# Kernel optimization log

Hardware: AMD Instinct MI355X
Metric: run time of the kernel (lower is better)

Reference implementation:

```python
import jax, jax.numpy as jnp
import numpy as np

N_EMBD = 768
NUM_EXPERTS = 64
EXPERT_WIDTH = 256            # all experts uniform width (expert_sizes=[(64,256)])
TOTAL_WIDTH = NUM_EXPERTS * EXPERT_WIDTH  # 16384
TOP_K = 8


def setup_inputs() -> dict:
    key = jax.random.key(0)
    k1, k2, k3, k4 = jax.random.split(key, 4)
    B, S = 1, 2048
    x = jax.random.normal(k1, (B, S, N_EMBD), dtype=jnp.float32)
    # router: nn.Linear(n_embd, num_experts, bias=False) -> weight [E, n_embd]
    router_w = jax.random.normal(k2, (NUM_EXPERTS, N_EMBD), dtype=jnp.float32) * 0.02
    # trunc_normal(std=0.02) approximated by clipped normal
    w1 = jnp.clip(jax.random.normal(k3, (N_EMBD, TOTAL_WIDTH), dtype=jnp.float32) * 0.02, -0.06, 0.06)
    w2 = jnp.clip(jax.random.normal(k4, (TOTAL_WIDTH, N_EMBD), dtype=jnp.float32) * 0.02, -0.06, 0.06)
    return {"x": x, "router_w": router_w, "w1": w1, "w2": w2}


def reference(x, router_w, w1, w2):
    B, S, D = x.shape
    T = B * S
    x_flat = x.reshape(T, D)

    # Router: sigmoid gating + top-k
    router_logits = x_flat @ router_w.T                      # [T, E]
    router_probs = jax.nn.sigmoid(router_logits.astype(jnp.float32))
    top_k_weights, selected_experts = jax.lax.top_k(router_probs, TOP_K)  # [T, K]
    top_k_weights = top_k_weights / (top_k_weights.sum(axis=-1, keepdims=True) + 1e-20)
    top_k_weights = top_k_weights.astype(x.dtype)

    # Per-token expert combine weights [T, E]: 0 for unselected experts.
    tok_idx = jnp.arange(T)[:, None]
    w_tok = jnp.zeros((T, NUM_EXPERTS), dtype=x.dtype).at[tok_idx, selected_experts].set(top_k_weights)

    # Expert MLP (relu^2 activation), dense-masked equivalent of
    # padded_gather -> grouped GEMM -> padded_scatter.
    h = jnp.square(jax.nn.relu(x_flat @ w1))                 # [T, E*W]
    h = (h.reshape(T, NUM_EXPERTS, EXPERT_WIDTH) * w_tok[:, :, None]).reshape(T, TOTAL_WIDTH)
    output = (h @ w2).reshape(B, S, D)

    # Aux losses
    router_z_loss = jnp.mean(jnp.square(jax.nn.logsumexp(router_logits, axis=-1)))
    tokens_per_expert = jnp.zeros((NUM_EXPERTS,), dtype=jnp.float32).at[selected_experts.reshape(-1)].add(1.0)
    f_i = (tokens_per_expert / tokens_per_expert.sum()).astype(x.dtype)
    p_i = router_probs.mean(axis=0)
    # all expert widths equal -> num_experts * (f_i . p_i)
    load_balance_loss = NUM_EXPERTS * (f_i.astype(jnp.float32) @ p_i)
    # expert_widths_normalized == ones -> mean over tokens of sum of probs
    compute_loss = router_probs.sum(axis=-1).mean()

    return output, router_z_loss, load_balance_loss, compute_loss, f_i
```

## Files before the change

kernel.cpp:

```cpp
#include <hip/hip_runtime.h>
#include <hip/hip_bf16.h>

#define T_TOKENS 2048
#define D_EMBD 768
#define N_EXP 64
#define EW 256
#define TOPK 8
#define TW (N_EXP*EW)
#define PAD_SLOTS 20480
#define SCHED_MAX 2560
#define OUT_BASE (2048*768)

typedef __attribute__((ext_vector_type(8))) short bf16x8;
typedef __attribute__((ext_vector_type(4))) float f32x4;

typedef __attribute__((address_space(1))) void GAS;
typedef __attribute__((address_space(3))) void LAS;
#define GLOAD16(g, l) __builtin_amdgcn_global_load_lds((GAS*)(g), (LAS*)(l), 16, 0, 0)

__device__ inline unsigned short f2bu(float f) {
  union { __hip_bfloat16 b; unsigned short u; } cv; cv.b = __float2bfloat16(f); return cv.u;
}
__device__ inline unsigned int pk2(float a, float b) {
  return (unsigned int)f2bu(a) | ((unsigned int)f2bu(b) << 16);
}

__global__ void k_init(int* counts, int* cursor, float* psum, float* scal,
                       float* wgt_slot, int* tok_slot, int* sched_e) {
  int i = blockIdx.x*256 + threadIdx.x;
  if (i < N_EXP) { counts[i] = 0; cursor[i] = 0; psum[i] = 0.f; }
  if (i < 2) scal[i] = 0.f;
  if (i < PAD_SLOTS) { wgt_slot[i] = 0.f; tok_slot[i] = 0; }
  if (i < SCHED_MAX) sched_e[i] = -1;
}

__global__ __launch_bounds__(256) void k_logits(const float* __restrict__ x,
                                                const float* __restrict__ rw,
                                                float* __restrict__ lp) {
  __shared__ float rw_s[8][256];
  int tid = threadIdx.x;
  int tg = blockIdx.x, eg = blockIdx.y, kc = blockIdx.z;
  #pragma unroll
  for (int idx = 0; idx < 8; idx++)
    rw_s[idx][tid] = rw[(size_t)(eg*8 + idx)*D_EMBD + kc*256 + tid];
  __syncthreads();
  int tok = tg*256 + tid;
  const float4* x4 = reinterpret_cast<const float4*>(x + (size_t)tok*D_EMBD + kc*256);
  float acc[8];
  #pragma unroll
  for (int e = 0; e < 8; e++) acc[e] = 0.f;
  #pragma unroll 4
  for (int k4 = 0; k4 < 64; k4++) {
    float4 xv = x4[k4];
    #pragma unroll
    for (int e = 0; e < 8; e++)
      acc[e] += xv.x*rw_s[e][k4*4+0] + xv.y*rw_s[e][k4*4+1]
              + xv.z*rw_s[e][k4*4+2] + xv.w*rw_s[e][k4*4+3];
  }
  float* dst = lp + (size_t)kc*T_TOKENS*N_EXP + (size_t)tok*N_EXP + eg*8;
  float4 o0 = {acc[0], acc[1], acc[2], acc[3]};
  float4 o1 = {acc[4], acc[5], acc[6], acc[7]};
  reinterpret_cast<float4*>(dst)[0] = o0;
  reinterpret_cast<float4*>(dst)[1] = o1;
}

__global__ __launch_bounds__(256) void k_router2(const float* __restrict__ lp,
                          int* __restrict__ sel_e, float* __restrict__ sel_w,
                          int* __restrict__ counts, float* __restrict__ psum,
                          float* __restrict__ scal) {
  __shared__ float psum_s[4][64];
  __shared__ int cnt_s[4][64];
  int tid = threadIdx.x, wv = tid >> 6, lane = tid & 63;
  float pacc = 0.f, zacc = 0.f;
  int cacc = 0;
  int tbase = blockIdx.x*8 + wv*2;
  #pragma unroll
  for (int it = 0; it < 2; it++) {
    int t = tbase + it;
    float logit = lp[(size_t)t*N_EXP + lane]
                + lp[(size_t)T_TOKENS*N_EXP + (size_t)t*N_EXP + lane]
                + lp[2*(size_t)T_TOKENS*N_EXP + (size_t)t*N_EXP + lane];
    float prob = 1.f/(1.f + expf(-logit));
    pacc += prob;
    float mx = logit;
    for (int s = 32; s; s >>= 1) mx = fmaxf(mx, __shfl_xor(mx, s, 64));
    float sse = expf(logit - mx);
    for (int s = 32; s; s >>= 1) sse += __shfl_xor(sse, s, 64);
    float lse = mx + logf(sse);
    zacc += lse*lse;
    int rank = 0;
    #pragma unroll
    for (int j = 0; j < 64; j++) {
      float pj = __shfl(prob, j, 64);
      rank += (pj > prob || (pj == prob && j < lane)) ? 1 : 0;
    }
    bool sel = rank < TOPK;
    float sp = sel ? prob : 0.f;
    for (int s = 32; s; s >>= 1) sp += __shfl_xor(sp, s, 64);
    if (sel) {
      sel_e[t*TOPK + rank] = lane;
      sel_w[t*TOPK + rank] = prob / (sp + 1e-20f);
      cacc++;
    }
  }
  psum_s[wv][lane] = pacc;
  cnt_s[wv][lane] = cacc;
  if (lane == 0) atomicAdd(&scal[0], zacc);
  __syncthreads();
  if (tid < 64) {
    float p = psum_s[0][tid] + psum_s[1][tid] + psum_s[2][tid] + psum_s[3][tid];
    int c = cnt_s[0][tid] + cnt_s[1][tid] + cnt_s[2][tid] + cnt_s[3][tid];
    atomicAdd(&psum[tid], p);
    atomicAdd(&counts[tid], c);
  }
}

__global__ void k_schedule(const int* __restrict__ counts, int* __restrict__ offsets,
                           int* __restrict__ sched_e, int* __restrict__ sched_r0) {
  int e = threadIdx.x;
  int c = counts[e];
  int tiles = (c + 63) >> 6;
  int padded = tiles << 6;
  int ip = padded;
  for (int s = 1; s < 64; s <<= 1) { int v = __shfl_up(ip, s, 64); if (e >= s) ip += v; }
  int rowoff = ip - padded;
  offsets[e] = rowoff;
  int it = tiles;
  for (int s = 8; s < 64; s <<= 1) { int v = __shfl_up(it, s, 64); if (e >= s) it += v; }
  int rank = it - tiles;
  int xcd = e & 7;
  for (int i = 0; i < tiles; i++) {
    int p = xcd + 8*(rank + i);
    sched_e[p] = e;
    sched_r0[p] = rowoff + i*64;
  }
}

__global__ void k_assign(const int* __restrict__ sel_e, const float* __restrict__ sel_w,
                         const int* __restrict__ offsets, int* __restrict__ cursor,
                         int* __restrict__ tok_slot, float* __restrict__ wgt_slot,
                         int* __restrict__ slot_tk) {
  int i = blockIdx.x*256 + threadIdx.x;
  int e = sel_e[i];
  int pos = atomicAdd(&cursor[e], 1);
  int slot = offsets[e] + pos;
  tok_slot[slot] = i >> 3;
  wgt_slot[slot] = sel_w[i];
  slot_tk[i] = slot;
}

template<int MODE>
__global__ __launch_bounds__(256) void k_moe_gemm(
    const void* __restrict__ Asrc, const float* __restrict__ Bsrc,
    const int* __restrict__ sched_e, const int* __restrict__ sched_r0,
    const int* __restrict__ tok_slot, const float* __restrict__ wgt_slot,
    __hip_bfloat16* __restrict__ outp) {
  constexpr int NS   = (MODE == 1) ? 12 : 4;
  constexpr int BSTR = (MODE == 1) ? TW : D_EMBD;
  __shared__ __hip_bfloat16 As[2][64*64];
  __shared__ __hip_bfloat16 Bs[2][128*64];
  int tid = threadIdx.x;
  int nch = blockIdx.y;
  int n4 = tid & 31, kpb = tid >> 5;
  int mrow = tid >> 4, k4f = tid & 15;
  int arl = tid >> 3, akc = tid & 7;
  int a_off = ((akc ^ (arl & 7)) << 3);
  int wv = tid >> 6, lane = tid & 63;
  int wm = wv >> 1, wn = wv & 1;
  int l15 = lane & 15, l4 = lane >> 4;

  for (int p = blockIdx.x; p < SCHED_MAX; p += gridDim.x) {
    int e = sched_e[p];
    if (e < 0) continue;
    int r0 = sched_r0[p];

    int browb = (MODE == 1) ? 0 : e*EW;
    int bcolb = (MODE == 1) ? (e*EW + nch*128) : nch*128;

    int tks[4];
    size_t a_base0 = 0, a_base1 = 0;
    if (MODE == 1) {
      #pragma unroll
      for (int i = 0; i < 4; i++) tks[i] = tok_slot[r0 + i*16 + mrow];
    } else {
      a_base0 = (size_t)(r0 + arl) * EW;
      a_base1 = (size_t)(r0 + arl + 32) * EW;
    }

    float bv[8][4], av[4][4];

    auto B_LOAD = [&](int k0) {
      const float* rp = Bsrc + (size_t)(browb + k0 + kpb*8)*BSTR + bcolb + n4*4;
      #pragma unroll
      for (int r = 0; r < 8; r++)
        *reinterpret_cast<float4*>(&bv[r][0]) =
            *reinterpret_cast<const float4*>(rp + (size_t)r*BSTR);
    };
    auto B_WRITE = [&](int bsel) {
      char* bs = (char*)&Bs[bsel][0];
      #pragma unroll
      for (int c = 0; c < 4; c++) {
        int n = n4*4 + c;
        int ch = kpb ^ ((n & 7) ^ ((n >> 3) & 7));
        uint4 o = { pk2(bv[0][c], bv[1][c]), pk2(bv[2][c], bv[3][c]),
                    pk2(bv[4][c], bv[5][c]), pk2(bv[6][c], bv[7][c]) };
        *reinterpret_cast<uint4*>(bs + n*128 + ch*16) = o;
      }
    };
    auto A_LOAD1 = [&](int k0) {
      const float* xf = (const float*)Asrc;
      #pragma unroll
      for (int i = 0; i < 4; i++)
        *reinterpret_cast<float4*>(&av[i][0]) =
            *reinterpret_cast<const float4*>(xf + (size_t)tks[i]*D_EMBD + k0 + k4f*4);
    };
    auto A_WRITE1 = [&](int bsel) {
      char* as_ = (char*)&As[bsel][0];
      #pragma unroll
      for (int i = 0; i < 4; i++) {
        int m = i*16 + mrow;
        int ch = (k4f >> 1) ^ (m & 7);
        uint2 val = { pk2(av[i][0], av[i][1]), pk2(av[i][2], av[i][3]) };
        *reinterpret_cast<uint2*>(as_ + m*128 + ch*16 + (k4f & 1)*8) = val;
      }
    };
    auto A_GLOAD2 = [&](int bsel, int k0) {
      const __hip_bfloat16* hb = (const __hip_bfloat16*)Asrc;
      GLOAD16(hb + a_base0 + k0 + a_off, &As[bsel][0] + tid*8);
      GLOAD16(hb + a_base1 + k0 + a_off, &As[bsel][0] + (256 + tid)*8);
    };

    f32x4 acc[2][4];
    f32x4 z = {0.f, 0.f, 0.f, 0.f};
    #pragma unroll
    for (int m = 0; m < 2; m++)
      #pragma unroll
      for (int n = 0; n < 4; n++) acc[m][n] = z;

    if (MODE == 1) { A_LOAD1(0); B_LOAD(0); A_WRITE1(0); B_WRITE(0); }
    else           { A_GLOAD2(0, 0); B_LOAD(0); B_WRITE(0);
                     asm volatile("s_waitcnt vmcnt(0)" ::: "memory"); }
    __syncthreads();

    int cur = 0;
    for (int step = 0; step < NS; step++) {
      bool more = (step + 1 < NS);
      int k1 = (step + 1)*64;
      if (more) {
        if (MODE == 1) { A_LOAD1(k1); B_LOAD(k1); }
        else           { A_GLOAD2(cur ^ 1, k1); B_LOAD(k1); }
      }
      const char* asC = (const char*)&As[cur][0];
      const char* bsC = (const char*)&Bs[cur][0];
      bf16x8 af[2][2], bq[4][2];
      #pragma unroll
      for (int m = 0; m < 2; m++) {
        int ra = wm*32 + m*16 + l15;
        #pragma unroll
        for (int kk = 0; kk < 2; kk++)
          af[m][kk] = *reinterpret_cast<const bf16x8*>(
              asC + ra*128 + (((kk*4 + l4) ^ (ra & 7)) << 4));
      }
      #pragma unroll
      for (int n = 0; n < 4; n++) {
        int rb = wn*64 + n*16 + l15;
        int Sb = (rb & 7) ^ ((rb >> 3) & 7);
        #pragma unroll
        for (int kk = 0; kk < 2; kk++)
          bq[n][kk] = *reinterpret_cast<const bf16x8*>(
              bsC + rb*128 + (((kk*4 + l4) ^ Sb) << 4));
      }
      #pragma unroll
      for (int kk = 0; kk < 2; kk++)
        #pragma unroll
        for (int m = 0; m < 2; m++)
          #pragma unroll
          for (int n = 0; n < 4; n++)
            acc[m][n] = __builtin_amdgcn_mfma_f32_16x16x32_bf16(af[m][kk], bq[n][kk], acc[m][n], 0, 0, 0);
      if (more) {
        if (MODE == 1) { A_WRITE1(cur ^ 1); B_WRITE(cur ^ 1); }
        else           { B_WRITE(cur ^ 1);
                         asm volatile("s_waitcnt vmcnt(0)" ::: "memory"); }
      }
      __syncthreads();
      cur ^= 1;
    }

    if (MODE == 1) {
      #pragma unroll
      for (int m = 0; m < 2; m++)
        #pragma unroll
        for (int j = 0; j < 4; j++) {
          int r = r0 + wm*32 + m*16 + l4*4 + j;
          float wg = wgt_slot[r];
          #pragma unroll
          for (int n = 0; n < 4; n++) {
            int col = nch*128 + wn*64 + n*16 + l15;
            float v = fmaxf(acc[m][n][j], 0.f);
            outp[(size_t)r*EW + col] = __float2bfloat16(v*v*wg);
          }
        }
    } else {
      #pragma unroll
      for (int m = 0; m < 2; m++)
        #pragma unroll
        for (int j = 0; j < 4; j++) {
          int r = r0 + wm*32 + m*16 + l4*4 + j;
          #pragma unroll
          for (int n = 0; n < 4; n++) {
            int col = nch*128 + wn*64 + n*16 + l15;
            outp[(size_t)r*D_EMBD + col] = __float2bfloat16(acc[m][n][j]);
          }
        }
    }
  }
}

__global__ void k_combine(const __hip_bfloat16* __restrict__ y, const int* __restrict__ slot_tk,
                          float* __restrict__ out) {
  __shared__ int s[TOPK];
  int t = blockIdx.x, tid = threadIdx.x;
  if (tid < TOPK) s[tid] = slot_tk[t*TOPK + tid];
  __syncthreads();
  if (tid < 192) {
    int c = tid*4;
    float a0 = 0.f, a1 = 0.f, a2 = 0.f, a3 = 0.f;
    #pragma unroll
    for (int k = 0; k < TOPK; k++) {
      ushort4 v = *reinterpret_cast<const ushort4*>(&y[(size_t)s[k]*D_EMBD + c]);
      union { unsigned int u; float f; } f0, f1, f2, f3;
      f0.u = ((unsigned int)v.x) << 16;
      f1.u = ((unsigned int)v.y) << 16;
      f2.u = ((unsigned int)v.z) << 16;
      f3.u = ((unsigned int)v.w) << 16;
      a0 += f0.f; a1 += f1.f; a2 += f2.f; a3 += f3.f;
    }
    float4 o = {a0, a1, a2, a3};
    *reinterpret_cast<float4*>(&out[(size_t)t*D_EMBD + c]) = o;
  }
}

__global__ void k_finalize(const int* __restrict__ counts, const float* __restrict__ psum,
                           const float* __restrict__ scal, float* __restrict__ out) {
  __shared__ float part[N_EXP], ptot[N_EXP];
  int e = threadIdx.x;
  float f = (float)counts[e] / 16384.f;
  float p = psum[e] / 2048.f;
  part[e] = f * p;
  ptot[e] = p;
  out[OUT_BASE + 3 + e] = f;
  __syncthreads();
  if (e == 0) {
    float s = 0.f, q = 0.f;
    for (int i = 0; i < N_EXP; i++) { s += part[i]; q += ptot[i]; }
    out[OUT_BASE + 0] = scal[0] / 2048.f;
    out[OUT_BASE + 1] = 64.f * s;
    out[OUT_BASE + 2] = q;
  }
}

extern "C" void kernel_launch(void* const* d_in, const int* in_sizes, int n_in,
                              void* d_out, int out_size, void* d_ws, size_t ws_size,
                              hipStream_t stream) {
  const float* x  = (const float*)d_in[0];
  const float* rw = (const float*)d_in[1];
  const float* w1 = (const float*)d_in[2];
  const float* w2 = (const float*)d_in[3];
  float* out = (float*)d_out;
  char* ws = (char*)d_ws;

  size_t o = 0;
  auto alloc = [&](size_t b) { size_t r = o; o += (b + 255) & ~(size_t)255; return r; };
  __hip_bfloat16* hprm  = (__hip_bfloat16*)(ws + alloc((size_t)PAD_SLOTS*256*2));
  __hip_bfloat16* yprm  = (__hip_bfloat16*)(ws + alloc((size_t)PAD_SLOTS*768*2));
  float* lp      = (float*)(ws + alloc(3UL*2048*64*4));
  int*   sel_e   = (int*)  (ws + alloc(16384UL*4));
  float* sel_w   = (float*)(ws + alloc(16384UL*4));
  int*   slot_tk = (int*)  (ws + alloc(16384UL*4));
  int*   tokslot = (int*)  (ws + alloc((size_t)PAD_SLOTS*4));
  float* wgtslot = (float*)(ws + alloc((size_t)PAD_SLOTS*4));
  int*   counts  = (int*)  (ws + alloc(256));
  int*   cursor  = (int*)  (ws + alloc(256));
  float* psum    = (float*)(ws + alloc(256));
  float* scal    = (float*)(ws + alloc(256));
  int*   offsets = (int*)  (ws + alloc(256));
  int*   sch_e   = (int*)  (ws + alloc(SCHED_MAX*4));
  int*   sch_r0  = (int*)  (ws + alloc(SCHED_MAX*4));

  k_init<<<80, 256, 0, stream>>>(counts, cursor, psum, scal, wgtslot, tokslot, sch_e);
  k_logits<<<dim3(8, 8, 3), 256, 0, stream>>>(x, rw, lp);
  k_router2<<<256, 256, 0, stream>>>(lp, sel_e, sel_w, counts, psum, scal);
  k_schedule<<<1, 64, 0, stream>>>(counts, offsets, sch_e, sch_r0);
  k_assign<<<64, 256, 0, stream>>>(sel_e, sel_w, offsets, cursor, tokslot, wgtslot, slot_tk);
  k_moe_gemm<1><<<dim3(512, 2), 256, 0, stream>>>((const void*)x, w1, sch_e, sch_r0, tokslot, wgtslot, hprm);
  k_moe_gemm<2><<<dim3(512, 6), 256, 0, stream>>>((const void*)hprm, w2, sch_e, sch_r0, tokslot, wgtslot, yprm);
  k_combine<<<2048, 256, 0, stream>>>(yprm, slot_tk, out);
  k_finalize<<<1, 64, 0, stream>>>(counts, psum, scal, out);
}
```

Before: 141.7 us.

## Deepen GEMM prefetch to two register stages and drop direct global-to-LDS loads

The MoE grouped-GEMM main loop now keeps two sets of register staging buffers, so global loads are issued two K-steps ahead while the current LDS tile is computed. The loop is manually unrolled by two and fully unrolled. The bf16 A-operand path now does ordinary register loads plus LDS stores instead of global_load_lds, which removes the blocking vmcnt(0) wait after each step. The cost is much higher register pressure, which may lower occupancy or cause spills.

```diff
diff --git a/kernel.cpp b/kernel.cpp
--- a/kernel.cpp
+++ b/kernel.cpp
@@ -13,10 +13,6 @@
 
 typedef __attribute__((ext_vector_type(8))) short bf16x8;
 typedef __attribute__((ext_vector_type(4))) float f32x4;
-
-typedef __attribute__((address_space(1))) void GAS;
-typedef __attribute__((address_space(3))) void LAS;
-#define GLOAD16(g, l) __builtin_amdgcn_global_load_lds((GAS*)(g), (LAS*)(l), 16, 0, 0)
 
 __device__ inline unsigned short f2bu(float f) {
   union { __hip_bfloat16 b; unsigned short u; } cv; cv.b = __float2bfloat16(f); return cv.u;
@@ -187,16 +183,18 @@
       a_base1 = (size_t)(r0 + arl + 32) * EW;
     }
 
-    float bv[8][4], av[4][4];
-
-    auto B_LOAD = [&](int k0) {
+    float av0[4][4], av1[4][4];
+    uint4 au0[2], au1[2];
+    float bv0_[8][4], bv1_[8][4];
+
+    auto B_LD = [&](float (&bv)[8][4], int k0) {
       const float* rp = Bsrc + (size_t)(browb + k0 + kpb*8)*BSTR + bcolb + n4*4;
       #pragma unroll
       for (int r = 0; r < 8; r++)
         *reinterpret_cast<float4*>(&bv[r][0]) =
             *reinterpret_cast<const float4*>(rp + (size_t)r*BSTR);
     };
-    auto B_WRITE = [&](int bsel) {
+    auto B_WR = [&](int bsel, float (&bv)[8][4]) {
       char* bs = (char*)&Bs[bsel][0];
       #pragma unroll
       for (int c = 0; c < 4; c++) {
@@ -207,14 +205,14 @@
         *reinterpret_cast<uint4*>(bs + n*128 + ch*16) = o;
       }
     };
-    auto A_LOAD1 = [&](int k0) {
+    auto A_LD1 = [&](float (&av)[4][4], int k0) {
       const float* xf = (const float*)Asrc;
       #pragma unroll
       for (int i = 0; i < 4; i++)
         *reinterpret_cast<float4*>(&av[i][0]) =
             *reinterpret_cast<const float4*>(xf + (size_t)tks[i]*D_EMBD + k0 + k4f*4);
     };
-    auto A_WRITE1 = [&](int bsel) {
+    auto A_WR1 = [&](int bsel, float (&av)[4][4]) {
       char* as_ = (char*)&As[bsel][0];
       #pragma unroll
       for (int i = 0; i < 4; i++) {
@@ -224,10 +222,15 @@
         *reinterpret_cast<uint2*>(as_ + m*128 + ch*16 + (k4f & 1)*8) = val;
       }
     };
-    auto A_GLOAD2 = [&](int bsel, int k0) {
+    auto A_LD2 = [&](uint4 (&au)[2], int k0) {
       const __hip_bfloat16* hb = (const __hip_bfloat16*)Asrc;
-      GLOAD16(hb + a_base0 + k0 + a_off, &As[bsel][0] + tid*8);
-      GLOAD16(hb + a_base1 + k0 + a_off, &As[bsel][0] + (256 + tid)*8);
+      au[0] = *reinterpret_cast<const uint4*>(hb + a_base0 + k0 + a_off);
+      au[1] = *reinterpret_cast<const uint4*>(hb + a_base1 + k0 + a_off);
+    };
+    auto A_WR2 = [&](int bsel, uint4 (&au)[2]) {
+      char* as_ = (char*)&As[bsel][0];
+      *reinterpret_cast<uint4*>(as_ + tid*16) = au[0];
+      *reinterpret_cast<uint4*>(as_ + 4096 + tid*16) = au[1];
     };
 
     f32x4 acc[2][4];
@@ -237,21 +240,9 @@
       #pragma unroll
       for (int n = 0; n < 4; n++) acc[m][n] = z;
 
-    if (MODE == 1) { A_LOAD1(0); B_LOAD(0); A_WRITE1(0); B_WRITE(0); }
-    else           { A_GLOAD2(0, 0); B_LOAD(0); B_WRITE(0);
-                     asm volatile("s_waitcnt vmcnt(0)" ::: "memory"); }
-    __syncthreads();
-
-    int cur = 0;
-    for (int step = 0; step < NS; step++) {
-      bool more = (step + 1 < NS);
-      int k1 = (step + 1)*64;
-      if (more) {
-        if (MODE == 1) { A_LOAD1(k1); B_LOAD(k1); }
-        else           { A_GLOAD2(cur ^ 1, k1); B_LOAD(k1); }
-      }
-      const char* asC = (const char*)&As[cur][0];
-      const char* bsC = (const char*)&Bs[cur][0];
+    auto COMPUTE = [&](int bsel) {
+      const char* asC = (const char*)&As[bsel][0];
+      const char* bsC = (const char*)&Bs[bsel][0];
       bf16x8 af[2][2], bq[4][2];
       #pragma unroll
       for (int m = 0; m < 2; m++) {
@@ -277,10 +268,38 @@
           #pragma unroll
           for (int n = 0; n < 4; n++)
             acc[m][n] = __builtin_amdgcn_mfma_f32_16x16x32_bf16(af[m][kk], bq[n][kk], acc[m][n], 0, 0, 0);
-      if (more) {
-        if (MODE == 1) { A_WRITE1(cur ^ 1); B_WRITE(cur ^ 1); }
-        else           { B_WRITE(cur ^ 1);
-                         asm volatile("s_waitcnt vmcnt(0)" ::: "memory"); }
+    };
+
+    if (MODE == 1) A_LD1(av0, 0); else A_LD2(au0, 0);
+    B_LD(bv0_, 0);
+    if (MODE == 1) A_LD1(av1, 64); else A_LD2(au1, 64);
+    B_LD(bv1_, 64);
+    if (MODE == 1) A_WR1(0, av0); else A_WR2(0, au0);
+    B_WR(0, bv0_);
+    __syncthreads();
+
+    int cur = 0;
+    #pragma unroll
+    for (int t = 0; t < NS; t += 2) {
+      if (t + 2 < NS) {
+        if (MODE == 1) A_LD1(av0, (t+2)*64); else A_LD2(au0, (t+2)*64);
+        B_LD(bv0_, (t+2)*64);
+      }
+      COMPUTE(cur);
+      if (t + 1 < NS) {
+        if (MODE == 1) A_WR1(cur ^ 1, av1); else A_WR2(cur ^ 1, au1);
+        B_WR(cur ^ 1, bv1_);
+      }
+      __syncthreads();
+      cur ^= 1;
+      if (t + 3 < NS) {
+        if (MODE == 1) A_LD1(av1, (t+3)*64); else A_LD2(au1, (t+3)*64);
+        B_LD(bv1_, (t+3)*64);
+      }
+      COMPUTE(cur);
+      if (t + 2 < NS) {
+        if (MODE == 1) A_WR1(cur ^ 1, av0); else A_WR2(cur ^ 1, au0);
+        B_WR(cur ^ 1, bv0_);
       }
       __syncthreads();
       cur ^= 1;
```

Result: slower. 149.7 us (+5.7%).

## Group expert tiles per XCD contiguously and replace LDS-direct loads with register staging

Applied to the files above, without the earlier changes.

The schedule now gives each group of eight experts a contiguous segment of GRP_POS slots. Each block handles slots from its XCD's segment, so one XCD processes whole experts and reuses their weights in its L2. The MODE 2 A-operand load no longer uses global_load_lds with an explicit vmcnt wait. It loads into registers and writes to LDS after the MFMAs, the same way the B path does. This may improve L2 locality and overlap, but load balance across XCDs now depends on routing skew between expert groups.

```diff
diff --git a/kernel.cpp b/kernel.cpp
--- a/kernel.cpp
+++ b/kernel.cpp
@@ -9,14 +9,11 @@
 #define TW (N_EXP*EW)
 #define PAD_SLOTS 20480
 #define SCHED_MAX 2560
+#define GRP_POS 320
 #define OUT_BASE (2048*768)
 
 typedef __attribute__((ext_vector_type(8))) short bf16x8;
 typedef __attribute__((ext_vector_type(4))) float f32x4;
-
-typedef __attribute__((address_space(1))) void GAS;
-typedef __attribute__((address_space(3))) void LAS;
-#define GLOAD16(g, l) __builtin_amdgcn_global_load_lds((GAS*)(g), (LAS*)(l), 16, 0, 0)
 
 __device__ inline unsigned short f2bu(float f) {
   union { __hip_bfloat16 b; unsigned short u; } cv; cv.b = __float2bfloat16(f); return cv.u;
@@ -126,11 +123,11 @@
   int rowoff = ip - padded;
   offsets[e] = rowoff;
   int it = tiles;
-  for (int s = 8; s < 64; s <<= 1) { int v = __shfl_up(it, s, 64); if (e >= s) it += v; }
+  for (int s = 1; s < 8; s <<= 1) { int v = __shfl_up(it, s, 64); if ((e & 7) >= s) it += v; }
   int rank = it - tiles;
-  int xcd = e & 7;
+  int grp = e >> 3;
   for (int i = 0; i < tiles; i++) {
-    int p = xcd + 8*(rank + i);
+    int p = grp*GRP_POS + rank + i;
     sched_e[p] = e;
     sched_r0[p] = rowoff + i*64;
   }
@@ -169,7 +166,10 @@
   int wm = wv >> 1, wn = wv & 1;
   int l15 = lane & 15, l4 = lane >> 4;
 
-  for (int p = blockIdx.x; p < SCHED_MAX; p += gridDim.x) {
+  int xcd = blockIdx.x & 7;
+  int q0 = blockIdx.x >> 3;
+  for (int q = q0; q < GRP_POS; q += 64) {
+    int p = xcd*GRP_POS + q;
     int e = sched_e[p];
     if (e < 0) continue;
     int r0 = sched_r0[p];
@@ -224,10 +224,17 @@
         *reinterpret_cast<uint2*>(as_ + m*128 + ch*16 + (k4f & 1)*8) = val;
       }
     };
-    auto A_GLOAD2 = [&](int bsel, int k0) {
+    auto A_LOAD2 = [&](int k0) {
       const __hip_bfloat16* hb = (const __hip_bfloat16*)Asrc;
-      GLOAD16(hb + a_base0 + k0 + a_off, &As[bsel][0] + tid*8);
-      GLOAD16(hb + a_base1 + k0 + a_off, &As[bsel][0] + (256 + tid)*8);
+      *reinterpret_cast<uint4*>(&av[0][0]) =
+          *reinterpret_cast<const uint4*>(hb + a_base0 + k0 + a_off);
+      *reinterpret_cast<uint4*>(&av[2][0]) =
+          *reinterpret_cast<const uint4*>(hb + a_base1 + k0 + a_off);
+    };
+    auto A_WRITE2 = [&](int bsel) {
+      char* as_ = (char*)&As[bsel][0];
+      *reinterpret_cast<uint4*>(as_ + tid*16) = *reinterpret_cast<uint4*>(&av[0][0]);
+      *reinterpret_cast<uint4*>(as_ + 4096 + tid*16) = *reinterpret_cast<uint4*>(&av[2][0]);
     };
 
     f32x4 acc[2][4];
@@ -238,8 +245,7 @@
       for (int n = 0; n < 4; n++) acc[m][n] = z;
 
     if (MODE == 1) { A_LOAD1(0); B_LOAD(0); A_WRITE1(0); B_WRITE(0); }
-    else           { A_GLOAD2(0, 0); B_LOAD(0); B_WRITE(0);
-                     asm volatile("s_waitcnt vmcnt(0)" ::: "memory"); }
+    else           { A_LOAD2(0); B_LOAD(0); A_WRITE2(0); B_WRITE(0); }
     __syncthreads();
 
     int cur = 0;
@@ -248,7 +254,7 @@
       int k1 = (step + 1)*64;
       if (more) {
         if (MODE == 1) { A_LOAD1(k1); B_LOAD(k1); }
-        else           { A_GLOAD2(cur ^ 1, k1); B_LOAD(k1); }
+        else           { A_LOAD2(k1); B_LOAD(k1); }
       }
       const char* asC = (const char*)&As[cur][0];
       const char* bsC = (const char*)&Bs[cur][0];
@@ -279,8 +285,7 @@
             acc[m][n] = __builtin_amdgcn_mfma_f32_16x16x32_bf16(af[m][kk], bq[n][kk], acc[m][n], 0, 0, 0);
       if (more) {
         if (MODE == 1) { A_WRITE1(cur ^ 1); B_WRITE(cur ^ 1); }
-        else           { B_WRITE(cur ^ 1);
-                         asm volatile("s_waitcnt vmcnt(0)" ::: "memory"); }
+        else           { A_WRITE2(cur ^ 1); B_WRITE(cur ^ 1); }
       }
       __syncthreads();
       cur ^= 1;
```

New measurement: 148.0 us. 1.04x slower.

## Enlarge MoE GEMM tiles to 256 rows and pre-convert x to bf16

Applied to the files above, without the earlier changes.

Each expert tile now covers 256 token rows with 512 threads, so the fp32 expert weights streamed from memory are reused across four times as many rows. The input x is converted to bf16 once up front, letting the first GEMM gather activations directly into LDS via async global-to-LDS loads. The schedule drops XCD interleaving and uses one block per tile instead of a persistent loop. Trade-offs are more padding waste per expert, fewer blocks to fill the GPU, and an extra conversion kernel.

```diff
diff --git a/kernel.cpp b/kernel.cpp
--- a/kernel.cpp
+++ b/kernel.cpp
@@ -7,8 +7,8 @@
 #define EW 256
 #define TOPK 8
 #define TW (N_EXP*EW)
-#define PAD_SLOTS 20480
-#define SCHED_MAX 2560
+#define PAD_SLOTS 32768
+#define SCHED_MAX 128
 #define OUT_BASE (2048*768)
 
 typedef __attribute__((ext_vector_type(8))) short bf16x8;
@@ -32,6 +32,14 @@
   if (i < 2) scal[i] = 0.f;
   if (i < PAD_SLOTS) { wgt_slot[i] = 0.f; tok_slot[i] = 0; }
   if (i < SCHED_MAX) sched_e[i] = -1;
+}
+
+__global__ void k_cvt_x(const float* __restrict__ x, __hip_bfloat16* __restrict__ xb) {
+  int i = blockIdx.x*256 + threadIdx.x;
+  float4 v = reinterpret_cast<const float4*>(x)[i];
+  ushort4 o;
+  o.x = f2bu(v.x); o.y = f2bu(v.y); o.z = f2bu(v.z); o.w = f2bu(v.w);
+  reinterpret_cast<ushort4*>(xb)[i] = o;
 }
 
 __global__ __launch_bounds__(256) void k_logits(const float* __restrict__ x,
@@ -119,20 +127,18 @@
                            int* __restrict__ sched_e, int* __restrict__ sched_r0) {
   int e = threadIdx.x;
   int c = counts[e];
-  int tiles = (c + 63) >> 6;
-  int padded = tiles << 6;
+  int tiles = (c + 255) >> 8;
+  int padded = tiles << 8;
   int ip = padded;
   for (int s = 1; s < 64; s <<= 1) { int v = __shfl_up(ip, s, 64); if (e >= s) ip += v; }
   int rowoff = ip - padded;
   offsets[e] = rowoff;
   int it = tiles;
-  for (int s = 8; s < 64; s <<= 1) { int v = __shfl_up(it, s, 64); if (e >= s) it += v; }
+  for (int s = 1; s < 64; s <<= 1) { int v = __shfl_up(it, s, 64); if (e >= s) it += v; }
   int rank = it - tiles;
-  int xcd = e & 7;
   for (int i = 0; i < tiles; i++) {
-    int p = xcd + 8*(rank + i);
-    sched_e[p] = e;
-    sched_r0[p] = rowoff + i*64;
+    sched_e[rank + i] = e;
+    sched_r0[rank + i] = rowoff + i*256;
   }
 }
 
@@ -150,169 +156,148 @@
 }
 
 template<int MODE>
-__global__ __launch_bounds__(256) void k_moe_gemm(
+__global__ __launch_bounds__(512) void k_moe_gemm(
     const void* __restrict__ Asrc, const float* __restrict__ Bsrc,
     const int* __restrict__ sched_e, const int* __restrict__ sched_r0,
     const int* __restrict__ tok_slot, const float* __restrict__ wgt_slot,
     __hip_bfloat16* __restrict__ outp) {
   constexpr int NS   = (MODE == 1) ? 12 : 4;
   constexpr int BSTR = (MODE == 1) ? TW : D_EMBD;
-  __shared__ __hip_bfloat16 As[2][64*64];
+  __shared__ __hip_bfloat16 As[2][256*64];
   __shared__ __hip_bfloat16 Bs[2][128*64];
   int tid = threadIdx.x;
   int nch = blockIdx.y;
-  int n4 = tid & 31, kpb = tid >> 5;
-  int mrow = tid >> 4, k4f = tid & 15;
+  int cp = tid & 63, ko = tid >> 6;
   int arl = tid >> 3, akc = tid & 7;
-  int a_off = ((akc ^ (arl & 7)) << 3);
+  int aoff = (akc ^ (arl & 7))*8;
   int wv = tid >> 6, lane = tid & 63;
   int wm = wv >> 1, wn = wv & 1;
   int l15 = lane & 15, l4 = lane >> 4;
 
-  for (int p = blockIdx.x; p < SCHED_MAX; p += gridDim.x) {
-    int e = sched_e[p];
-    if (e < 0) continue;
-    int r0 = sched_r0[p];
-
-    int browb = (MODE == 1) ? 0 : e*EW;
-    int bcolb = (MODE == 1) ? (e*EW + nch*128) : nch*128;
-
-    int tks[4];
-    size_t a_base0 = 0, a_base1 = 0;
-    if (MODE == 1) {
-      #pragma unroll
-      for (int i = 0; i < 4; i++) tks[i] = tok_slot[r0 + i*16 + mrow];
-    } else {
-      a_base0 = (size_t)(r0 + arl) * EW;
-      a_base1 = (size_t)(r0 + arl + 32) * EW;
-    }
-
-    float bv[8][4], av[4][4];
-
-    auto B_LOAD = [&](int k0) {
-      const float* rp = Bsrc + (size_t)(browb + k0 + kpb*8)*BSTR + bcolb + n4*4;
-      #pragma unroll
-      for (int r = 0; r < 8; r++)
-        *reinterpret_cast<float4*>(&bv[r][0]) =
-            *reinterpret_cast<const float4*>(rp + (size_t)r*BSTR);
-    };
-    auto B_WRITE = [&](int bsel) {
-      char* bs = (char*)&Bs[bsel][0];
-      #pragma unroll
-      for (int c = 0; c < 4; c++) {
-        int n = n4*4 + c;
-        int ch = kpb ^ ((n & 7) ^ ((n >> 3) & 7));
-        uint4 o = { pk2(bv[0][c], bv[1][c]), pk2(bv[2][c], bv[3][c]),
-                    pk2(bv[4][c], bv[5][c]), pk2(bv[6][c], bv[7][c]) };
-        *reinterpret_cast<uint4*>(bs + n*128 + ch*16) = o;
+  int p = blockIdx.x;
+  int e = sched_e[p];
+  if (e < 0) return;
+  int r0 = sched_r0[p];
+
+  size_t brow0 = (MODE == 1) ? 0 : (size_t)e*EW;
+  int bcol = (MODE == 1) ? (e*EW + nch*128) : nch*128;
+
+  size_t abase[4];
+  #pragma unroll
+  for (int i = 0; i < 4; i++) {
+    if (MODE == 1) abase[i] = (size_t)tok_slot[r0 + i*64 + arl] * D_EMBD;
+    else           abase[i] = (size_t)(r0 + i*64 + arl) * EW;
+  }
+
+  float2 bv[8];
+
+  auto B_LD = [&](int k0) {
+    const float* rp = Bsrc + (brow0 + k0 + ko*8)*BSTR + bcol + cp*2;
+    #pragma unroll
+    for (int r = 0; r < 8; r++)
+      bv[r] = *reinterpret_cast<const float2*>(rp + (size_t)r*BSTR);
+  };
+  auto B_WR = [&](int bsel) {
+    char* bs = (char*)&Bs[bsel][0];
+    #pragma unroll
+    for (int c = 0; c < 2; c++) {
+      int n = cp*2 + c;
+      int ch = ko ^ ((n & 7) ^ ((n >> 3) & 7));
+      float v0 = c ? bv[0].y : bv[0].x, v1 = c ? bv[1].y : bv[1].x;
+      float v2 = c ? bv[2].y : bv[2].x, v3 = c ? bv[3].y : bv[3].x;
+      float v4 = c ? bv[4].y : bv[4].x, v5 = c ? bv[5].y : bv[5].x;
+      float v6 = c ? bv[6].y : bv[6].x, v7 = c ? bv[7].y : bv[7].x;
+      uint4 o = { pk2(v0, v1), pk2(v2, v3), pk2(v4, v5), pk2(v6, v7) };
+      *reinterpret_cast<uint4*>(bs + n*128 + ch*16) = o;
+    }
+  };
+  auto A_ST = [&](int bsel, int k0) {
+    const __hip_bfloat16* ab = (const __hip_bfloat16*)Asrc;
+    #pragma unroll
+    for (int i = 0; i < 4; i++)
+      GLOAD16(ab + abase[i] + k0 + aoff, &As[bsel][0] + (i*512 + tid)*8);
+  };
+
+  f32x4 acc[4][4];
+  f32x4 z = {0.f, 0.f, 0.f, 0.f};
+  #pragma unroll
+  for (int m = 0; m < 4; m++)
+    #pragma unroll
+    for (int n = 0; n < 4; n++) acc[m][n] = z;
+
+  auto COMPUTE = [&](int bsel) {
+    const char* asC = (const char*)&As[bsel][0];
+    const char* bsC = (const char*)&Bs[bsel][0];
+    bf16x8 af[4][2], bq[4][2];
+    #pragma unroll
+    for (int m = 0; m < 4; m++) {
+      int ra = wm*64 + m*16 + l15;
+      #pragma unroll
+      for (int kk = 0; kk < 2; kk++)
+        af[m][kk] = *reinterpret_cast<const bf16x8*>(
+            asC + ra*128 + (((kk*4 + l4) ^ (ra & 7)) << 4));
+    }
+    #pragma unroll
+    for (int n = 0; n < 4; n++) {
+      int rb = wn*64 + n*16 + l15;
+      int Sb = (rb & 7) ^ ((rb >> 3) & 7);
+      #pragma unroll
+      for (int kk = 0; kk < 2; kk++)
+        bq[n][kk] = *reinterpret_cast<const bf16x8*>(
+            bsC + rb*128 + (((kk*4 + l4) ^ Sb) << 4));
+    }
+    #pragma unroll
+    for (int kk = 0; kk < 2; kk++)
+      #pragma unroll
+      for (int m = 0; m < 4; m++)
+        #pragma unroll
+        for (int n = 0; n < 4; n++)
+          acc[m][n] = __builtin_amdgcn_mfma_f32_16x16x32_bf16(af[m][kk], bq[n][kk], acc[m][n], 0, 0, 0);
+  };
+
+  A_ST(0, 0);
+  B_LD(0);
+  B_WR(0);
+  asm volatile("s_waitcnt vmcnt(0)" ::: "memory");
+  __syncthreads();
+
+  int cur = 0;
+  for (int step = 0; step < NS; step++) {
+    bool more = (step + 1 < NS);
+    if (more) { A_ST(cur ^ 1, (step + 1)*64); B_LD((step + 1)*64); }
+    COMPUTE(cur);
+    if (more) B_WR(cur ^ 1);
+    asm volatile("s_waitcnt vmcnt(0)" ::: "memory");
+    __syncthreads();
+    cur ^= 1;
+  }
+
+  if (MODE == 1) {
+    #pragma unroll
+    for (int m = 0; m < 4; m++)
+      #pragma unroll
+      for (int j = 0; j < 4; j++) {
+        int r = r0 + wm*64 + m*16 + l4*4 + j;
+        float wg = wgt_slot[r];
+        #pragma unroll
+        for (int n = 0; n < 4; n++) {
+          int col = nch*128 + wn*64 + n*16 + l15;
+          float v = fmaxf(acc[m][n][j], 0.f);
+          outp[(size_t)r*EW + col] = __float2bfloat16(v*v*wg);
+        }
       }
-    };
-    auto A_LOAD1 = [&](int k0) {
-      const float* xf = (const float*)Asrc;
-      #pragma unroll
-      for (int i = 0; i < 4; i++)
-        *reinterpret_cast<float4*>(&av[i][0]) =
-            *reinterpret_cast<const float4*>(xf + (size_t)tks[i]*D_EMBD + k0 + k4f*4);
-    };
-    auto A_WRITE1 = [&](int bsel) {
-      char* as_ = (char*)&As[bsel][0];
-      #pragma unroll
-      for (int i = 0; i < 4; i++) {
-        int m = i*16 + mrow;
-        int ch = (k4f >> 1) ^ (m & 7);
-        uint2 val = { pk2(av[i][0], av[i][1]), pk2(av[i][2], av[i][3]) };
-        *reinterpret_cast<uint2*>(as_ + m*128 + ch*16 + (k4f & 1)*8) = val;
+  } else {
+    #pragma unroll
+    for (int m = 0; m < 4; m++)
+      #pragma unroll
+      for (int j = 0; j < 4; j++) {
+        int r = r0 + wm*64 + m*16 + l4*4 + j;
+        #pragma unroll
+        for (int n = 0; n < 4; n++) {
+          int col = nch*128 + wn*64 + n*16 + l15;
+          outp[(size_t)r*D_EMBD + col] = __float2bfloat16(acc[m][n][j]);
+        }
       }
-    };
-    auto A_GLOAD2 = [&](int bsel, int k0) {
-      const __hip_bfloat16* hb = (const __hip_bfloat16*)Asrc;
-      GLOAD16(hb + a_base0 + k0 + a_off, &As[bsel][0] + tid*8);
-      GLOAD16(hb + a_base1 + k0 + a_off, &As[bsel][0] + (256 + tid)*8);
-    };
-
-    f32x4 acc[2][4];
-    f32x4 z = {0.f, 0.f, 0.f, 0.f};
-    #pragma unroll
-    for (int m = 0; m < 2; m++)
-      #pragma unroll
-      for (int n = 0; n < 4; n++) acc[m][n] = z;
-
-    if (MODE == 1) { A_LOAD1(0); B_LOAD(0); A_WRITE1(0); B_WRITE(0); }
-    else           { A_GLOAD2(0, 0); B_LOAD(0); B_WRITE(0);
-                     asm volatile("s_waitcnt vmcnt(0)" ::: "memory"); }
-    __syncthreads();
-
-    int cur = 0;
-    for (int step = 0; step < NS; step++) {
-      bool more = (step + 1 < NS);
-      int k1 = (step + 1)*64;
-      if (more) {
-        if (MODE == 1) { A_LOAD1(k1); B_LOAD(k1); }
-        else           { A_GLOAD2(cur ^ 1, k1); B_LOAD(k1); }
-      }
-      const char* asC = (const char*)&As[cur][0];
-      const char* bsC = (const char*)&Bs[cur][0];
-      bf16x8 af[2][2], bq[4][2];
-      #pragma unroll
-      for (int m = 0; m < 2; m++) {
-        int ra = wm*32 + m*16 + l15;
-        #pragma unroll
-        for (int kk = 0; kk < 2; kk++)
-          af[m][kk] = *reinterpret_cast<const bf16x8*>(
-              asC + ra*128 + (((kk*4 + l4) ^ (ra & 7)) << 4));
-      }
-      #pragma unroll
-      for (int n = 0; n < 4; n++) {
-        int rb = wn*64 + n*16 + l15;
-        int Sb = (rb & 7) ^ ((rb >> 3) & 7);
-        #pragma unroll
-        for (int kk = 0; kk < 2; kk++)
-          bq[n][kk] = *reinterpret_cast<const bf16x8*>(
-              bsC + rb*128 + (((kk*4 + l4) ^ Sb) << 4));
-      }
-      #pragma unroll
-      for (int kk = 0; kk < 2; kk++)
-        #pragma unroll
-        for (int m = 0; m < 2; m++)
-          #pragma unroll
-          for (int n = 0; n < 4; n++)
-            acc[m][n] = __builtin_amdgcn_mfma_f32_16x16x32_bf16(af[m][kk], bq[n][kk], acc[m][n], 0, 0, 0);
-      if (more) {
-        if (MODE == 1) { A_WRITE1(cur ^ 1); B_WRITE(cur ^ 1); }
-        else           { B_WRITE(cur ^ 1);
-                         asm volatile("s_waitcnt vmcnt(0)" ::: "memory"); }
-      }
-      __syncthreads();
-      cur ^= 1;
-    }
-
-    if (MODE == 1) {
-      #pragma unroll
-      for (int m = 0; m < 2; m++)
-        #pragma unroll
-        for (int j = 0; j < 4; j++) {
-          int r = r0 + wm*32 + m*16 + l4*4 + j;
-          float wg = wgt_slot[r];
-          #pragma unroll
-          for (int n = 0; n < 4; n++) {
-            int col = nch*128 + wn*64 + n*16 + l15;
-            float v = fmaxf(acc[m][n][j], 0.f);
-            outp[(size_t)r*EW + col] = __float2bfloat16(v*v*wg);
-          }
-        }
-    } else {
-      #pragma unroll
-      for (int m = 0; m < 2; m++)
-        #pragma unroll
-        for (int j = 0; j < 4; j++) {
-          int r = r0 + wm*32 + m*16 + l4*4 + j;
-          #pragma unroll
-          for (int n = 0; n < 4; n++) {
-            int col = nch*128 + wn*64 + n*16 + l15;
-            outp[(size_t)r*D_EMBD + col] = __float2bfloat16(acc[m][n][j]);
-          }
-        }
-    }
   }
 }
 
@@ -371,6 +356,7 @@
 
   size_t o = 0;
   auto alloc = [&](size_t b) { size_t r = o; o += (b + 255) & ~(size_t)255; return r; };
+  __hip_bfloat16* xb    = (__hip_bfloat16*)(ws + alloc(2048UL*768*2));
   __hip_bfloat16* hprm  = (__hip_bfloat16*)(ws + alloc((size_t)PAD_SLOTS*256*2));
   __hip_bfloat16* yprm  = (__hip_bfloat16*)(ws + alloc((size_t)PAD_SLOTS*768*2));
   float* lp      = (float*)(ws + alloc(3UL*2048*64*4));
@@ -387,13 +373,14 @@
   int*   sch_e   = (int*)  (ws + alloc(SCHED_MAX*4));
   int*   sch_r0  = (int*)  (ws + alloc(SCHED_MAX*4));
 
-  k_init<<<80, 256, 0, stream>>>(counts, cursor, psum, scal, wgtslot, tokslot, sch_e);
+  k_init<<<128, 256, 0, stream>>>(counts, cursor, psum, scal, wgtslot, tokslot, sch_e);
+  k_cvt_x<<<1536, 256, 0, stream>>>(x, xb);
   k_logits<<<dim3(8, 8, 3), 256, 0, stream>>>(x, rw, lp);
   k_router2<<<256, 256, 0, stream>>>(lp, sel_e, sel_w, counts, psum, scal);
   k_schedule<<<1, 64, 0, stream>>>(counts, offsets, sch_e, sch_r0);
   k_assign<<<64, 256, 0, stream>>>(sel_e, sel_w, offsets, cursor, tokslot, wgtslot, slot_tk);
-  k_moe_gemm<1><<<dim3(512, 2), 256, 0, stream>>>((const void*)x, w1, sch_e, sch_r0, tokslot, wgtslot, hprm);
-  k_moe_gemm<2><<<dim3(512, 6), 256, 0, stream>>>((const void*)hprm, w2, sch_e, sch_r0, tokslot, wgtslot, yprm);
+  k_moe_gemm<1><<<dim3(SCHED_MAX, 2), 512, 0, stream>>>((const void*)xb, w1, sch_e, sch_r0, tokslot, wgtslot, hprm);
+  k_moe_gemm<2><<<dim3(SCHED_MAX, 6), 512, 0, stream>>>((const void*)hprm, w2, sch_e, sch_r0, tokslot, wgtslot, yprm);
   k_combine<<<2048, 256, 0, stream>>>(yprm, slot_tk, out);
   k_finalize<<<1, 64, 0, stream>>>(counts, psum, scal, out);
 }
```

Result: slower. 145.0 us (+2.3%).
